# Optimization experiments

Measured on AMD Instinct MI355X. Metric: run time of the kernel, lower is better.

Reference implementation:

```python
import jax, jax.numpy as jnp
import numpy as np

NEG_INF = -1e9

def setup_inputs() -> dict:
    key = jax.random.key(0)
    k1, k2, k3, k4, k5 = jax.random.split(key, 5)
    N, F_IN, F_OUT, H = 8192, 128, 32, 4
    node_features = jax.random.normal(k1, (N, F_IN), dtype=jnp.float32)
    adj_matrix = jax.random.randint(k2, (N, N), 0, 2, dtype=jnp.int32)
    # stacked per-head params (original: one Linear W [F_IN,F_OUT] + attention vec a [2*F_OUT] per head)
    W = jax.random.normal(k3, (H, F_IN, F_OUT), dtype=jnp.float32) * (1.0 / np.sqrt(F_IN))
    a_src = jax.random.normal(k4, (H, F_OUT), dtype=jnp.float32) * 0.1
    a_dst = jax.random.normal(k5, (H, F_OUT), dtype=jnp.float32) * 0.1
    return {"node_features": node_features, "adj_matrix": adj_matrix,
            "W": W, "a_src": a_src, "a_dst": a_dst}

def reference(node_features, adj_matrix, W, a_src, a_dst):
    alpha = 0.2  # LeakyReLU negative slope
    # project: [H, N, F_OUT]
    h = jnp.einsum('nf,hfo->hno', node_features, W)
    # GAT scores e_ij = LeakyReLU(a_src . h_i + a_dst . h_j), shape [H, N, N]
    e_src = jnp.einsum('hno,ho->hn', h, a_src)  # [H, N]
    e_dst = jnp.einsum('hno,ho->hn', h, a_dst)  # [H, N]
    e = jax.nn.leaky_relu(e_src[:, :, None] + e_dst[:, None, :], negative_slope=alpha)
    mask = (adj_matrix > 0)[None, :, :]
    attn = jax.nn.softmax(jnp.where(mask, e, NEG_INF), axis=-1)  # [H, N, N]
    out = jnp.einsum('hij,hjo->hio', attn, h)  # [H, N, F_OUT]
    # concat heads along feature dim -> [N, H*F_OUT]
    H_, N_, O_ = out.shape
    return jnp.transpose(out, (1, 0, 2)).reshape(N_, H_ * O_)
```

## Files before the change

kernel.cpp:

```cpp
#include <hip/hip_runtime.h>
#include <hip/hip_bf16.h>

#define NTOT 8192
#define FIN 128
#define FOUT 32
#define NH 4
#define NSEG 4
#define SEGJ (NTOT / NSEG)
#define LOG2E 1.4426950408889634f

typedef __attribute__((ext_vector_type(4))) float f32x4;
typedef __attribute__((ext_vector_type(4))) int i32x4;
typedef __attribute__((ext_vector_type(4))) unsigned int u32x4;
typedef __attribute__((ext_vector_type(8))) __bf16 bf16x8;
typedef unsigned long long u64;
typedef unsigned int u32;

__device__ __forceinline__ unsigned short f2bf(float x) {
  __hip_bfloat16 h = __float2bfloat16(x);
  return *reinterpret_cast<unsigned short*>(&h);
}

__device__ __forceinline__ float fexp2(float y) {
  float p;
  asm("v_exp_f32 %0, %1" : "=v"(p) : "v"(y));
  return p;
}

__global__ __launch_bounds__(256, 2) void k1_project(
    const float* __restrict__ X, const float* __restrict__ W,
    float* __restrict__ h, unsigned short* __restrict__ panel) {
  __shared__ float Xs[32 * 128];
  __shared__ float Ws[32 * 128];
  __shared__ unsigned short Hs[128 * 40];
  int t = threadIdx.x;
  int nb = blockIdx.x * 32;

  const f32x4* Xg = reinterpret_cast<const f32x4*>(X + (size_t)nb * FIN);
  f32x4* Xs4 = reinterpret_cast<f32x4*>(Xs);
#pragma unroll
  for (int r = 0; r < 4; ++r) Xs4[t + r * 256] = Xg[t + r * 256];

  int ng = t >> 5, oq = t & 31;
  int n0 = ng * 4, o0 = oq * 4;
  f32x4 acc[4];
#pragma unroll
  for (int nn = 0; nn < 4; ++nn) acc[nn] = (f32x4){0.f, 0.f, 0.f, 0.f};

  for (int kp = 0; kp < 4; ++kp) {
    __syncthreads();
#pragma unroll
    for (int r = 0; r < 4; ++r) {
      int q = t + r * 256;
      int flat = q * 4;
      int kk = flat >> 7;
      int c = flat & 127;
      int hdd = c >> 5;
      int oo = c & 31;
      *reinterpret_cast<f32x4*>(&Ws[kk * 128 + c]) =
          *reinterpret_cast<const f32x4*>(W + hdd * (FIN * FOUT) +
                                          (kp * 32 + kk) * FOUT + oo);
    }
    __syncthreads();
#pragma unroll 8
    for (int kk = 0; kk < 32; ++kk) {
      f32x4 wv = *reinterpret_cast<const f32x4*>(&Ws[kk * 128 + o0]);
#pragma unroll
      for (int nn = 0; nn < 4; ++nn)
        acc[nn] += Xs[(n0 + nn) * 128 + kp * 32 + kk] * wv;
    }
  }
#pragma unroll
  for (int nn = 0; nn < 4; ++nn) {
    *reinterpret_cast<f32x4*>(&h[(size_t)(nb + n0 + nn) * 128 + o0]) = acc[nn];
#pragma unroll
    for (int c = 0; c < 4; ++c)
      Hs[(o0 + c) * 40 + (n0 + nn)] = f2bf(acc[nn][c]);
  }
  __syncthreads();
  int jt = blockIdx.x;
#pragma unroll
  for (int it = 0; it < 2; ++it) {
    int item = t + it * 256;
    int p = item >> 6;
    int l = item & 63;
    int o = p * 16 + (l & 15);
    u32x4 v = *reinterpret_cast<const u32x4*>(&Hs[o * 40 + (l >> 4) * 8]);
    *reinterpret_cast<u32x4*>(panel + (size_t)(p * 256 + jt) * 512 + l * 8) = v;
  }
}

__global__ __launch_bounds__(256, 2) void k2_scores(
    const float* __restrict__ h, const float* __restrict__ a_src,
    const float* __restrict__ a_dst, float* __restrict__ Sl2,
    float* __restrict__ Dt) {
  int n = blockIdx.x * 256 + threadIdx.x;
  const f32x4* hv = reinterpret_cast<const f32x4*>(h + (size_t)n * 128);
  const f32x4* as4 = reinterpret_cast<const f32x4*>(a_src);
  const f32x4* ad4 = reinterpret_cast<const f32x4*>(a_dst);
#pragma unroll
  for (int hd = 0; hd < NH; ++hd) {
    f32x4 sa = {0.f, 0.f, 0.f, 0.f}, da = {0.f, 0.f, 0.f, 0.f};
#pragma unroll
    for (int q = 0; q < 8; ++q) {
      f32x4 x = hv[hd * 8 + q];
      sa += x * as4[hd * 8 + q];
      da += x * ad4[hd * 8 + q];
    }
    float s = (sa[0] + sa[1]) + (sa[2] + sa[3]);
    float d = (da[0] + da[1]) + (da[2] + da[3]);
    Sl2[hd * NTOT + n] = s * LOG2E;
    Dt[(n >> 6) * 256 + hd * 64 + (n & 63)] = d * LOG2E;
  }
}

__global__ __launch_bounds__(256)
__attribute__((amdgpu_waves_per_eu(2, 2))) void k3_attn(
    const int* __restrict__ adj, const float* __restrict__ Sl2,
    const float* __restrict__ Dt, const unsigned short* __restrict__ panel,
    float* __restrict__ pacc, float* __restrict__ plsum) {
  const int N = NTOT;
  int tid = threadIdx.x;
  int w = tid >> 6, l = tid & 63;
  int itile = blockIdx.x >> 2, seg = blockIdx.x & 3;
  int ibase = itile * 64;
  int m = l & 15, g = l >> 4, jc = g * 8;
  int row = ibase + w * 16 + m;
  int seg0 = seg * 32;

  float svv[4];
#pragma unroll
  for (int hd = 0; hd < 4; ++hd) svv[hd] = Sl2[hd * N + row];

  const int* adjr = adj + (size_t)row * N + seg * SEGJ + jc;

  f32x4 z4 = {0.f, 0.f, 0.f, 0.f};
  f32x4 c0[4] = {z4, z4, z4, z4}, c1[4] = {z4, z4, z4, z4},
        cs[4] = {z4, z4, z4, z4};
  bf16x8 bones;
  {
    u32 pat = (m == 0) ? 0x3f803f80u : 0u;
    u32x4 tmp = {pat, pat, pat, pat};
    bones = *reinterpret_cast<bf16x8*>(&tmp);
  }

  i32x4 Aa0, Aa1, Aa2, Aa3, Ba0, Ba1, Ba2, Ba3;

#define AISS(P, t_)                                            \
  {                                                            \
    int tc_ = (t_) > 31 ? 31 : (t_);                           \
    const int* a_ = adjr + tc_ * 64;                           \
    P##a0 = *reinterpret_cast<const i32x4*>(a_);               \
    P##a1 = *reinterpret_cast<const i32x4*>(a_ + 4);           \
    P##a2 = *reinterpret_cast<const i32x4*>(a_ + 32);          \
    P##a3 = *reinterpret_cast<const i32x4*>(a_ + 36);          \
  }                                                            \
  __builtin_amdgcn_sched_barrier(0);

#define AFSEL(AF, AV0, AV1, DA, DB, SV)                                  \
  {                                                                      \
    f32x4 xa_ = (DA) + (SV);                                             \
    f32x4 xb_ = (DB) + (SV);                                             \
    f32x4 ya_ = __builtin_elementwise_max(xa_, 0.2f * xa_);              \
    f32x4 yb_ = __builtin_elementwise_max(xb_, 0.2f * xb_);              \
    _Pragma("unroll") for (int e = 0; e < 4; ++e) {                      \
      float y_ = ((AV0)[e] != 0) ? ya_[e] : -1e9f;                       \
      AF[e] = (__bf16)fexp2(y_);                                         \
    }                                                                    \
    _Pragma("unroll") for (int e = 0; e < 4; ++e) {                      \
      float y_ = ((AV1)[e] != 0) ? yb_[e] : -1e9f;                       \
      AF[e + 4] = (__bf16)fexp2(y_);                                     \
    }                                                                    \
  }

#define MFM(AF, B, ACC) \
  ACC = __builtin_amdgcn_mfma_f32_16x16x32_bf16(AF, B, ACC, 0, 0, 0);

#define MATHM(P, t_)                                                       \
  {                                                                       \
    int jm_ = seg0 + (t_);                                                \
    const float* db_ = Dt + (size_t)jm_ * 256;                            \
    const unsigned short* pb_ =                                           \
        panel + (size_t)(seg * 64 + (t_)*2) * 512 + l * 8;                \
    _Pragma("unroll") for (int hd = 0; hd < 4; ++hd) {                    \
      f32x4 d0 = *(const f32x4*)(db_ + hd * 64 + jc);                     \
      f32x4 d1 = *(const f32x4*)(db_ + hd * 64 + jc + 4);                 \
      f32x4 d2 = *(const f32x4*)(db_ + hd * 64 + 32 + jc);                \
      f32x4 d3 = *(const f32x4*)(db_ + hd * 64 + 32 + jc + 4);            \
      const unsigned short* p0_ = pb_ + (size_t)(hd * 2) * 131072;        \
      const unsigned short* p1_ = pb_ + (size_t)(hd * 2 + 1) * 131072;    \
      bf16x8 B0a = *(const bf16x8*)(p0_);                                 \
      bf16x8 B1a = *(const bf16x8*)(p1_);                                 \
      bf16x8 B0b = *(const bf16x8*)(p0_ + 512);                           \
      bf16x8 B1b = *(const bf16x8*)(p1_ + 512);                           \
      float sv_ = svv[hd];                                                \
      bf16x8 af_;                                                         \
      AFSEL(af_, P##a0, P##a1, d0, d1, sv_)                               \
      MFM(af_, B0a, c0[hd]) MFM(af_, B1a, c1[hd]) MFM(af_, bones, cs[hd]) \
      AFSEL(af_, P##a2, P##a3, d2, d3, sv_)                               \
      MFM(af_, B0b, c0[hd]) MFM(af_, B1b, c1[hd]) MFM(af_, bones, cs[hd]) \
    }                                                                     \
  }

  AISS(A, 0)
  AISS(B, 1)
#pragma unroll 1
  for (int tt = 0; tt < 16; ++tt) {
    MATHM(A, 2 * tt)
    AISS(A, 2 * tt + 2)
    MATHM(B, 2 * tt + 1)
    AISS(B, 2 * tt + 3)
  }
#undef AISS
#undef AFSEL
#undef MFM
#undef MATHM

#pragma unroll
  for (int hd = 0; hd < 4; ++hd) {
    int rb = ibase + w * 16 + g * 4;
    if (m == 0) {
#pragma unroll
      for (int r = 0; r < 4; ++r)
        plsum[(seg * NH + hd) * N + rb + r] = cs[hd][r];
    }
#pragma unroll
    for (int r = 0; r < 4; ++r) {
      int rowr = rb + r;
      pacc[((size_t)seg * N + rowr) * 128 + hd * 32 + m] = c0[hd][r];
      pacc[((size_t)seg * N + rowr) * 128 + hd * 32 + 16 + m] = c1[hd][r];
    }
  }
}

__global__ __launch_bounds__(256, 2) void k4_combine(
    const float* __restrict__ pacc, const float* __restrict__ plsum,
    float* __restrict__ out) {
  int idx = blockIdx.x * 256 + threadIdx.x;
  int i = idx >> 7;
  int c = idx & 127;
  int hd = c >> 5;
  float a = 0.f, ls = 0.f;
#pragma unroll
  for (int s = 0; s < NSEG; ++s) {
    a += pacc[((size_t)s * NTOT + i) * 128 + c];
    ls += plsum[(s * NH + hd) * NTOT + i];
  }
  out[idx] = (ls > 0.f) ? a / ls : 0.f;
}

extern "C" void kernel_launch(void* const* d_in, const int* in_sizes, int n_in,
                              void* d_out, int out_size, void* d_ws,
                              size_t ws_size, hipStream_t stream) {
  const float* X = (const float*)d_in[0];
  const int* adj = (const int*)d_in[1];
  const float* W = (const float*)d_in[2];
  const float* a_src = (const float*)d_in[3];
  const float* a_dst = (const float*)d_in[4];
  float* out = (float*)d_out;

  char* ws = (char*)d_ws;
  float* h = (float*)(ws + 0x0);
  unsigned short* panel = (unsigned short*)(ws + 0x400000);
  float* Sl2 = (float*)(ws + 0x600000);
  float* Dt = (float*)(ws + 0x620000);
  float* pacc = (float*)(ws + 0xE40000);
  float* plsum = (float*)(ws + 0x1E40000);

  k1_project<<<dim3(256), dim3(256), 0, stream>>>(X, W, h, panel);
  k2_scores<<<dim3(32), dim3(256), 0, stream>>>(h, a_src, a_dst, Sl2, Dt);
  k3_attn<<<dim3(128 * NSEG), dim3(256), 0, stream>>>(adj, Sl2, Dt, panel,
                                                      pacc, plsum);
  k4_combine<<<dim3(4096), dim3(256), 0, stream>>>(pacc, plsum, out);
}
```

Baseline: 146.5 us.

## Factor exp of LeakyReLU scores into separable row/column terms, removing per-element exp

Rewrites exp(leakyrelu(s_i+d_j)) as either exp(s_i)·exp(d_j) or exp(0.2 s_i)·exp(0.2 d_j), chosen per element by the sign of s_i+d_j. The column factors are precomputed in bf16 and the row factors are applied once after accumulation. The attention kernel then only selects and masks bit patterns and runs two MFMA accumulator sets, so the per-element transcendental disappears. It also changes the work split: each wave handles two heads over 16 rows, with twice as many blocks, and the occupancy constraint is relaxed. The costs are doubled MFMA work, the sign test running on bf16-rounded d, no max-subtraction (so exp overflow is possible for large scores), and the adjacency matrix being re-read once per head pair.

New measurement: 170.4 us. +16.4%, slower.

```diff
diff --git a/kernel.cpp b/kernel.cpp
--- a/kernel.cpp
+++ b/kernel.cpp
@@ -7,7 +7,6 @@
 #define NH 4
 #define NSEG 4
 #define SEGJ (NTOT / NSEG)
-#define LOG2E 1.4426950408889634f
 
 typedef __attribute__((ext_vector_type(4))) float f32x4;
 typedef __attribute__((ext_vector_type(4))) int i32x4;
@@ -19,12 +18,6 @@
 __device__ __forceinline__ unsigned short f2bf(float x) {
   __hip_bfloat16 h = __float2bfloat16(x);
   return *reinterpret_cast<unsigned short*>(&h);
-}
-
-__device__ __forceinline__ float fexp2(float y) {
-  float p;
-  asm("v_exp_f32 %0, %1" : "=v"(p) : "v"(y));
-  return p;
 }
 
 __global__ __launch_bounds__(256, 2) void k1_project(
@@ -92,12 +85,15 @@
 
 __global__ __launch_bounds__(256, 2) void k2_scores(
     const float* __restrict__ h, const float* __restrict__ a_src,
-    const float* __restrict__ a_dst, float* __restrict__ Sl2,
-    float* __restrict__ Dt) {
+    const float* __restrict__ a_dst, float* __restrict__ Sf,
+    float* __restrict__ E1f, float* __restrict__ E2f,
+    unsigned short* __restrict__ Dbf, unsigned short* __restrict__ F1bf,
+    unsigned short* __restrict__ F2bf) {
   int n = blockIdx.x * 256 + threadIdx.x;
   const f32x4* hv = reinterpret_cast<const f32x4*>(h + (size_t)n * 128);
   const f32x4* as4 = reinterpret_cast<const f32x4*>(a_src);
   const f32x4* ad4 = reinterpret_cast<const f32x4*>(a_dst);
+  int jm = n >> 6, jo = n & 63;
 #pragma unroll
   for (int hd = 0; hd < NH; ++hd) {
     f32x4 sa = {0.f, 0.f, 0.f, 0.f}, da = {0.f, 0.f, 0.f, 0.f};
@@ -109,34 +105,52 @@
     }
     float s = (sa[0] + sa[1]) + (sa[2] + sa[3]);
     float d = (da[0] + da[1]) + (da[2] + da[3]);
-    Sl2[hd * NTOT + n] = s * LOG2E;
-    Dt[(n >> 6) * 256 + hd * 64 + (n & 63)] = d * LOG2E;
+    Sf[hd * NTOT + n] = s;
+    E1f[hd * NTOT + n] = expf(s);
+    E2f[hd * NTOT + n] = expf(0.2f * s);
+    int ti = (jm * 4 + hd) * 64 + jo;
+    Dbf[ti] = f2bf(d);
+    F1bf[ti] = f2bf(expf(d));
+    F2bf[ti] = f2bf(expf(0.2f * d));
   }
 }
 
 __global__ __launch_bounds__(256)
-__attribute__((amdgpu_waves_per_eu(2, 2))) void k3_attn(
-    const int* __restrict__ adj, const float* __restrict__ Sl2,
-    const float* __restrict__ Dt, const unsigned short* __restrict__ panel,
-    float* __restrict__ pacc, float* __restrict__ plsum) {
+__attribute__((amdgpu_waves_per_eu(2))) void k3_attn(
+    const int* __restrict__ adj, const float* __restrict__ Sf,
+    const float* __restrict__ E1f, const float* __restrict__ E2f,
+    const unsigned short* __restrict__ Dbf,
+    const unsigned short* __restrict__ F1bf,
+    const unsigned short* __restrict__ F2bf,
+    const unsigned short* __restrict__ panel, float* __restrict__ pacc,
+    float* __restrict__ plsum) {
   const int N = NTOT;
   int tid = threadIdx.x;
   int w = tid >> 6, l = tid & 63;
+  int rh = w & 1, hp = w >> 1;
   int itile = blockIdx.x >> 2, seg = blockIdx.x & 3;
-  int ibase = itile * 64;
+  int ibase = itile * 32 + rh * 16;
   int m = l & 15, g = l >> 4, jc = g * 8;
-  int row = ibase + w * 16 + m;
-  int seg0 = seg * 32;
-
-  float svv[4];
-#pragma unroll
-  for (int hd = 0; hd < 4; ++hd) svv[hd] = Sl2[hd * N + row];
+  int row = ibase + m;
+  int hd0 = hp * 2;
+
+  float sv0 = Sf[hd0 * N + row];
+  float sv1 = Sf[(hd0 + 1) * N + row];
 
   const int* adjr = adj + (size_t)row * N + seg * SEGJ + jc;
+  const char* dB =
+      (const char*)Dbf + (size_t)(seg * 32) * 512 + hd0 * 128 + jc * 2;
+  const char* f1B =
+      (const char*)F1bf + (size_t)(seg * 32) * 512 + hd0 * 128 + jc * 2;
+  const char* f2B =
+      (const char*)F2bf + (size_t)(seg * 32) * 512 + hd0 * 128 + jc * 2;
+  const char* pB = (const char*)panel +
+                   ((size_t)(hd0 * 2) * 256 + seg * 64) * 1024 + (size_t)l * 16;
+  const size_t PS = (size_t)256 * 1024;
 
   f32x4 z4 = {0.f, 0.f, 0.f, 0.f};
-  f32x4 c0[4] = {z4, z4, z4, z4}, c1[4] = {z4, z4, z4, z4},
-        cs[4] = {z4, z4, z4, z4};
+  f32x4 aP0[2] = {z4, z4}, aP1[2] = {z4, z4}, aPs[2] = {z4, z4};
+  f32x4 aN0[2] = {z4, z4}, aN1[2] = {z4, z4}, aNs[2] = {z4, z4};
   bf16x8 bones;
   {
     u32 pat = (m == 0) ? 0x3f803f80u : 0u;
@@ -144,91 +158,92 @@
     bones = *reinterpret_cast<bf16x8*>(&tmp);
   }
 
-  i32x4 Aa0, Aa1, Aa2, Aa3, Ba0, Ba1, Ba2, Ba3;
-
-#define AISS(P, t_)                                            \
-  {                                                            \
-    int tc_ = (t_) > 31 ? 31 : (t_);                           \
-    const int* a_ = adjr + tc_ * 64;                           \
-    P##a0 = *reinterpret_cast<const i32x4*>(a_);               \
-    P##a1 = *reinterpret_cast<const i32x4*>(a_ + 4);           \
-    P##a2 = *reinterpret_cast<const i32x4*>(a_ + 32);          \
-    P##a3 = *reinterpret_cast<const i32x4*>(a_ + 36);          \
-  }                                                            \
-  __builtin_amdgcn_sched_barrier(0);
-
-#define AFSEL(AF, AV0, AV1, DA, DB, SV)                                  \
-  {                                                                      \
-    f32x4 xa_ = (DA) + (SV);                                             \
-    f32x4 xb_ = (DB) + (SV);                                             \
-    f32x4 ya_ = __builtin_elementwise_max(xa_, 0.2f * xa_);              \
-    f32x4 yb_ = __builtin_elementwise_max(xb_, 0.2f * xb_);              \
-    _Pragma("unroll") for (int e = 0; e < 4; ++e) {                      \
-      float y_ = ((AV0)[e] != 0) ? ya_[e] : -1e9f;                       \
-      AF[e] = (__bf16)fexp2(y_);                                         \
-    }                                                                    \
-    _Pragma("unroll") for (int e = 0; e < 4; ++e) {                      \
-      float y_ = ((AV1)[e] != 0) ? yb_[e] : -1e9f;                       \
-      AF[e + 4] = (__bf16)fexp2(y_);                                     \
-    }                                                                    \
-  }
-
 #define MFM(AF, B, ACC) \
   ACC = __builtin_amdgcn_mfma_f32_16x16x32_bf16(AF, B, ACC, 0, 0, 0);
 
-#define MATHM(P, t_)                                                       \
+#define AFPLANE(HH, MK, Dv, F1v, F2v, B0, B1, SV)                         \
   {                                                                       \
-    int jm_ = seg0 + (t_);                                                \
-    const float* db_ = Dt + (size_t)jm_ * 256;                            \
-    const unsigned short* pb_ =                                           \
-        panel + (size_t)(seg * 64 + (t_)*2) * 512 + l * 8;                \
-    _Pragma("unroll") for (int hd = 0; hd < 4; ++hd) {                    \
-      f32x4 d0 = *(const f32x4*)(db_ + hd * 64 + jc);                     \
-      f32x4 d1 = *(const f32x4*)(db_ + hd * 64 + jc + 4);                 \
-      f32x4 d2 = *(const f32x4*)(db_ + hd * 64 + 32 + jc);                \
-      f32x4 d3 = *(const f32x4*)(db_ + hd * 64 + 32 + jc + 4);            \
-      const unsigned short* p0_ = pb_ + (size_t)(hd * 2) * 131072;        \
-      const unsigned short* p1_ = pb_ + (size_t)(hd * 2 + 1) * 131072;    \
-      bf16x8 B0a = *(const bf16x8*)(p0_);                                 \
-      bf16x8 B1a = *(const bf16x8*)(p1_);                                 \
-      bf16x8 B0b = *(const bf16x8*)(p0_ + 512);                           \
-      bf16x8 B1b = *(const bf16x8*)(p1_ + 512);                           \
-      float sv_ = svv[hd];                                                \
-      bf16x8 af_;                                                         \
-      AFSEL(af_, P##a0, P##a1, d0, d1, sv_)                               \
-      MFM(af_, B0a, c0[hd]) MFM(af_, B1a, c1[hd]) MFM(af_, bones, cs[hd]) \
-      AFSEL(af_, P##a2, P##a3, d2, d3, sv_)                               \
-      MFM(af_, B0b, c0[hd]) MFM(af_, B1b, c1[hd]) MFM(af_, bones, cs[hd]) \
+    u32x4 aPw, aNw;                                                       \
+    _Pragma("unroll") for (int p = 0; p < 4; ++p) {                       \
+      float de = __uint_as_float(Dv[p] << 16);                            \
+      float dodd = __uint_as_float(Dv[p] & 0xFFFF0000u);                  \
+      u32 n0 = (u32)(__float_as_int((SV) + de) >> 31);                    \
+      u32 n1 = (u32)(__float_as_int((SV) + dodd) >> 31);                  \
+      u32 mn = __builtin_amdgcn_perm(n1, n0, 0x05040100u);                \
+      aPw[p] = F1v[p] & ((MK)[p] & ~mn);                                  \
+      aNw[p] = F2v[p] & ((MK)[p] & mn);                                   \
     }                                                                     \
-  }
-
-  AISS(A, 0)
-  AISS(B, 1)
+    bf16x8 afP = *reinterpret_cast<bf16x8*>(&aPw);                        \
+    bf16x8 afN = *reinterpret_cast<bf16x8*>(&aNw);                        \
+    MFM(afP, B0, aP0[HH]) MFM(afP, B1, aP1[HH]) MFM(afP, bones, aPs[HH])  \
+    MFM(afN, B0, aN0[HH]) MFM(afN, B1, aN1[HH]) MFM(afN, bones, aNs[HH])  \
+  }
+
 #pragma unroll 1
-  for (int tt = 0; tt < 16; ++tt) {
-    MATHM(A, 2 * tt)
-    AISS(A, 2 * tt + 2)
-    MATHM(B, 2 * tt + 1)
-    AISS(B, 2 * tt + 3)
-  }
-#undef AISS
-#undef AFSEL
+  for (int t = 0; t < 32; ++t) {
+    const int* a_ = adjr + t * 64;
+    i32x4 a0 = *reinterpret_cast<const i32x4*>(a_);
+    i32x4 a1 = *reinterpret_cast<const i32x4*>(a_ + 4);
+    i32x4 a2 = *reinterpret_cast<const i32x4*>(a_ + 32);
+    i32x4 a3 = *reinterpret_cast<const i32x4*>(a_ + 36);
+    u32x4 mkA, mkB;
+#pragma unroll
+    for (int p = 0; p < 2; ++p) {
+      mkA[p] = __builtin_amdgcn_perm((u32)(-a0[2 * p + 1]), (u32)(-a0[2 * p]),
+                                     0x05040100u);
+      mkA[p + 2] = __builtin_amdgcn_perm((u32)(-a1[2 * p + 1]),
+                                         (u32)(-a1[2 * p]), 0x05040100u);
+      mkB[p] = __builtin_amdgcn_perm((u32)(-a2[2 * p + 1]), (u32)(-a2[2 * p]),
+                                     0x05040100u);
+      mkB[p + 2] = __builtin_amdgcn_perm((u32)(-a3[2 * p + 1]),
+                                         (u32)(-a3[2 * p]), 0x05040100u);
+    }
+    size_t tb = (size_t)t * 512;
+    size_t pb = (size_t)t * 2048;
+#pragma unroll
+    for (int hh = 0; hh < 2; ++hh) {
+      float sv_ = hh ? sv1 : sv0;
+      const char* d_ = dB + tb + hh * 128;
+      const char* f1_ = f1B + tb + hh * 128;
+      const char* f2_ = f2B + tb + hh * 128;
+      const char* p0_ = pB + pb + (size_t)(hh * 2) * PS;
+      const char* p1_ = p0_ + PS;
+      {
+        u32x4 Dv = *(const u32x4*)(d_);
+        u32x4 F1v = *(const u32x4*)(f1_);
+        u32x4 F2v = *(const u32x4*)(f2_);
+        bf16x8 B0 = *(const bf16x8*)(p0_);
+        bf16x8 B1 = *(const bf16x8*)(p1_);
+        AFPLANE(hh, mkA, Dv, F1v, F2v, B0, B1, sv_)
+      }
+      {
+        u32x4 Dv = *(const u32x4*)(d_ + 64);
+        u32x4 F1v = *(const u32x4*)(f1_ + 64);
+        u32x4 F2v = *(const u32x4*)(f2_ + 64);
+        bf16x8 B0 = *(const bf16x8*)(p0_ + 1024);
+        bf16x8 B1 = *(const bf16x8*)(p1_ + 1024);
+        AFPLANE(hh, mkB, Dv, F1v, F2v, B0, B1, sv_)
+      }
+    }
+  }
+#undef AFPLANE
 #undef MFM
-#undef MATHM
-
-#pragma unroll
-  for (int hd = 0; hd < 4; ++hd) {
-    int rb = ibase + w * 16 + g * 4;
-    if (m == 0) {
-#pragma unroll
-      for (int r = 0; r < 4; ++r)
-        plsum[(seg * NH + hd) * N + rb + r] = cs[hd][r];
-    }
+
+#pragma unroll
+  for (int hh = 0; hh < 2; ++hh) {
+    int hd = hd0 + hh;
+    int rb = ibase + g * 4;
 #pragma unroll
     for (int r = 0; r < 4; ++r) {
       int rowr = rb + r;
-      pacc[((size_t)seg * N + rowr) * 128 + hd * 32 + m] = c0[hd][r];
-      pacc[((size_t)seg * N + rowr) * 128 + hd * 32 + 16 + m] = c1[hd][r];
+      float e1 = E1f[hd * N + rowr], e2 = E2f[hd * N + rowr];
+      if (m == 0)
+        plsum[(seg * NH + hd) * N + rowr] =
+            e1 * aPs[hh][r] + e2 * aNs[hh][r];
+      pacc[((size_t)seg * N + rowr) * 128 + hd * 32 + m] =
+          e1 * aP0[hh][r] + e2 * aN0[hh][r];
+      pacc[((size_t)seg * N + rowr) * 128 + hd * 32 + 16 + m] =
+          e1 * aP1[hh][r] + e2 * aN1[hh][r];
     }
   }
 }
@@ -262,14 +277,19 @@
   char* ws = (char*)d_ws;
   float* h = (float*)(ws + 0x0);
   unsigned short* panel = (unsigned short*)(ws + 0x400000);
-  float* Sl2 = (float*)(ws + 0x600000);
-  float* Dt = (float*)(ws + 0x620000);
-  float* pacc = (float*)(ws + 0xE40000);
-  float* plsum = (float*)(ws + 0x1E40000);
+  float* Sf = (float*)(ws + 0x600000);
+  float* E1f = (float*)(ws + 0x620000);
+  float* E2f = (float*)(ws + 0x640000);
+  unsigned short* Dbf = (unsigned short*)(ws + 0x660000);
+  unsigned short* F1bf = (unsigned short*)(ws + 0x670000);
+  unsigned short* F2bf = (unsigned short*)(ws + 0x680000);
+  float* pacc = (float*)(ws + 0x700000);
+  float* plsum = (float*)(ws + 0x1700000);
 
   k1_project<<<dim3(256), dim3(256), 0, stream>>>(X, W, h, panel);
-  k2_scores<<<dim3(32), dim3(256), 0, stream>>>(h, a_src, a_dst, Sl2, Dt);
-  k3_attn<<<dim3(128 * NSEG), dim3(256), 0, stream>>>(adj, Sl2, Dt, panel,
-                                                      pacc, plsum);
+  k2_scores<<<dim3(32), dim3(256), 0, stream>>>(h, a_src, a_dst, Sf, E1f, E2f,
+                                                Dbf, F1bf, F2bf);
+  k3_attn<<<dim3(256 * NSEG), dim3(256), 0, stream>>>(
+      adj, Sf, E1f, E2f, Dbf, F1bf, F2bf, panel, pacc, plsum);
   k4_combine<<<dim3(4096), dim3(256), 0, stream>>>(pacc, plsum, out);
 }
```

## Stage adjacency tiles into LDS via async global_load_lds with swizzle

Applied to the files above, without the earlier changes.

Replaces the per-lane direct register loads of the int32 adjacency rows with per-wave asynchronous global-to-LDS DMA copies of 16-row by 1KB chunks, using an XOR swizzle so that each wave's loads are contiguous and coalesced. Each staged chunk is then read back from LDS in a layout that avoids bank conflicts. The wave waits for all loads before computing, so the next chunk's transfer overlaps only with earlier work, not within the compute. It adds 64KB of LDS per block, which may limit occupancy, and it relaxes the waves_per_eu upper bound. Workspace offsets for pacc and plsum are also moved.

After: 155.7 us. +6.3%, slower.

```diff
diff --git a/kernel.cpp b/kernel.cpp
--- a/kernel.cpp
+++ b/kernel.cpp
@@ -25,6 +25,12 @@
   float p;
   asm("v_exp_f32 %0, %1" : "=v"(p) : "v"(y));
   return p;
+}
+
+__device__ __forceinline__ void dma16(const void* g, void* l) {
+  __builtin_amdgcn_global_load_lds(
+      (const __attribute__((address_space(1))) void*)g,
+      (__attribute__((address_space(3))) void*)l, 16, 0, 0);
 }
 
 __global__ __launch_bounds__(256, 2) void k1_project(
@@ -115,11 +121,12 @@
 }
 
 __global__ __launch_bounds__(256)
-__attribute__((amdgpu_waves_per_eu(2, 2))) void k3_attn(
+__attribute__((amdgpu_waves_per_eu(2))) void k3_attn(
     const int* __restrict__ adj, const float* __restrict__ Sl2,
     const float* __restrict__ Dt, const unsigned short* __restrict__ panel,
     float* __restrict__ pacc, float* __restrict__ plsum) {
   const int N = NTOT;
+  __shared__ char adjS[4 * 16384];
   int tid = threadIdx.x;
   int w = tid >> 6, l = tid & 63;
   int itile = blockIdx.x >> 2, seg = blockIdx.x & 3;
@@ -132,7 +139,10 @@
 #pragma unroll
   for (int hd = 0; hd < 4; ++hd) svv[hd] = Sl2[hd * N + row];
 
-  const int* adjr = adj + (size_t)row * N + seg * SEGJ + jc;
+  char* myS = adjS + w * 16384;
+  const char* adjB =
+      (const char*)adj + ((size_t)(ibase + w * 16) * N + seg * SEGJ) * 4;
+  int lsw = l * 16;
 
   f32x4 z4 = {0.f, 0.f, 0.f, 0.f};
   f32x4 c0[4] = {z4, z4, z4, z4}, c1[4] = {z4, z4, z4, z4},
@@ -144,18 +154,14 @@
     bones = *reinterpret_cast<bf16x8*>(&tmp);
   }
 
-  i32x4 Aa0, Aa1, Aa2, Aa3, Ba0, Ba1, Ba2, Ba3;
-
-#define AISS(P, t_)                                            \
-  {                                                            \
-    int tc_ = (t_) > 31 ? 31 : (t_);                           \
-    const int* a_ = adjr + tc_ * 64;                           \
-    P##a0 = *reinterpret_cast<const i32x4*>(a_);               \
-    P##a1 = *reinterpret_cast<const i32x4*>(a_ + 4);           \
-    P##a2 = *reinterpret_cast<const i32x4*>(a_ + 32);          \
-    P##a3 = *reinterpret_cast<const i32x4*>(a_ + 36);          \
-  }                                                            \
-  __builtin_amdgcn_sched_barrier(0);
+#define STAGE(sup_)                                                      \
+  {                                                                      \
+    _Pragma("unroll") for (int i = 0; i < 16; ++i) {                     \
+      const char* g_ = adjB + (size_t)i * (N * 4) + (sup_)*1024 +        \
+                       (size_t)(lsw ^ ((i & 7) << 4));                   \
+      dma16(g_, myS + i * 1024);                                         \
+    }                                                                    \
+  }
 
 #define AFSEL(AF, AV0, AV1, DA, DB, SV)                                  \
   {                                                                      \
@@ -176,7 +182,7 @@
 #define MFM(AF, B, ACC) \
   ACC = __builtin_amdgcn_mfma_f32_16x16x32_bf16(AF, B, ACC, 0, 0, 0);
 
-#define MATHM(P, t_)                                                       \
+#define MATHM(t_, A0, A1, A2, A3)                                         \
   {                                                                       \
     int jm_ = seg0 + (t_);                                                \
     const float* db_ = Dt + (size_t)jm_ * 256;                            \
@@ -195,23 +201,35 @@
       bf16x8 B1b = *(const bf16x8*)(p1_ + 512);                           \
       float sv_ = svv[hd];                                                \
       bf16x8 af_;                                                         \
-      AFSEL(af_, P##a0, P##a1, d0, d1, sv_)                               \
+      AFSEL(af_, A0, A1, d0, d1, sv_)                                     \
       MFM(af_, B0a, c0[hd]) MFM(af_, B1a, c1[hd]) MFM(af_, bones, cs[hd]) \
-      AFSEL(af_, P##a2, P##a3, d2, d3, sv_)                               \
+      AFSEL(af_, A2, A3, d2, d3, sv_)                                     \
       MFM(af_, B0b, c0[hd]) MFM(af_, B1b, c1[hd]) MFM(af_, bones, cs[hd]) \
     }                                                                     \
   }
 
-  AISS(A, 0)
-  AISS(B, 1)
+  STAGE(0)
+  int swz = (m & 7) << 4;
+  const char* rb_ = myS + m * 1024;
+
 #pragma unroll 1
-  for (int tt = 0; tt < 16; ++tt) {
-    MATHM(A, 2 * tt)
-    AISS(A, 2 * tt + 2)
-    MATHM(B, 2 * tt + 1)
-    AISS(B, 2 * tt + 3)
-  }
-#undef AISS
+  for (int sup = 0; sup < 8; ++sup) {
+    asm volatile("s_waitcnt vmcnt(0)" ::: "memory");
+    __builtin_amdgcn_sched_barrier(0);
+#pragma unroll
+    for (int mm = 0; mm < 4; ++mm) {
+      int base_ = mm * 256 + g * 32;
+      i32x4 a0 = *(const i32x4*)(rb_ + ((base_ + 0) ^ swz));
+      i32x4 a1 = *(const i32x4*)(rb_ + ((base_ + 16) ^ swz));
+      i32x4 a2 = *(const i32x4*)(rb_ + ((base_ + 128) ^ swz));
+      i32x4 a3 = *(const i32x4*)(rb_ + ((base_ + 144) ^ swz));
+      MATHM(sup * 4 + mm, a0, a1, a2, a3)
+    }
+    asm volatile("s_waitcnt lgkmcnt(0)" ::: "memory");
+    __builtin_amdgcn_sched_barrier(0);
+    if (sup < 7) STAGE(sup + 1)
+  }
+#undef STAGE
 #undef AFSEL
 #undef MFM
 #undef MATHM
@@ -264,8 +282,8 @@
   unsigned short* panel = (unsigned short*)(ws + 0x400000);
   float* Sl2 = (float*)(ws + 0x600000);
   float* Dt = (float*)(ws + 0x620000);
-  float* pacc = (float*)(ws + 0xE40000);
-  float* plsum = (float*)(ws + 0x1E40000);
+  float* pacc = (float*)(ws + 0x700000);
+  float* plsum = (float*)(ws + 0x1700000);
 
   k1_project<<<dim3(256), dim3(256), 0, stream>>>(X, W, h, panel);
   k2_scores<<<dim3(32), dim3(256), 0, stream>>>(h, a_src, a_dst, Sl2, Dt);
```
